# Kernel optimization log

Measured on AMD Instinct MI355X. Metric: run time of the kernel, lower is better.

The kernel has to match this reference:

```python
import jax, jax.numpy as jnp
import numpy as np

B, T, M, D, H, DFF = 8, 512, 64, 1024, 16, 4096
DH = D // H          # 64 head dim
ROT = DH // 2        # 32 rotary dims (int(head_dim*0.5))
ROPE_BASE = 10000.0
LN_EPS = 1e-5


def layernorm(x, g, b):
    mu = jnp.mean(x, -1, keepdims=True)
    var = jnp.mean(jnp.square(x - mu), -1, keepdims=True)
    return (x - mu) * jax.lax.rsqrt(var + LN_EPS) * g + b


def rotate_half(x):
    x1, x2 = x[..., : x.shape[-1] // 2], x[..., x.shape[-1] // 2:]
    return jnp.concatenate((-x2, x1), -1)


def setup_inputs() -> dict:
    key = jax.random.key(0)
    ks = jax.random.split(key, 8)
    s = 0.02
    return {
        "x": jax.random.normal(ks[0], (B, T, D), jnp.float32),
        "memory": jax.random.normal(ks[1], (B, M, D), jnp.float32),
        "Wq": jax.random.normal(ks[2], (D, D), jnp.float32) * s,
        "bq": jnp.zeros((D,), jnp.float32),
        "Wk": jax.random.normal(ks[3], (D, D), jnp.float32) * s,
        "bk": jnp.zeros((D,), jnp.float32),
        "Wv": jax.random.normal(ks[4], (D, D), jnp.float32) * s,
        "bv": jnp.zeros((D,), jnp.float32),
        "Wo": jax.random.normal(ks[5], (D, D), jnp.float32) * s,
        "bo": jnp.zeros((D,), jnp.float32),
        "W1": jax.random.normal(ks[6], (DFF, D), jnp.float32) * s,
        "b1": jnp.zeros((DFF,), jnp.float32),
        "W2": jax.random.normal(ks[7], (D, DFF), jnp.float32) * s,
        "b2": jnp.zeros((D,), jnp.float32),
        "g_attn": jnp.ones((D,), jnp.float32),
        "beta_attn": jnp.zeros((D,), jnp.float32),
        "g_mlp": jnp.ones((D,), jnp.float32),
        "beta_mlp": jnp.zeros((D,), jnp.float32),
    }


def reference(x, memory, Wq, bq, Wk, bk, Wv, bv, Wo, bo, W1, b1, W2, b2,
              g_attn, beta_attn, g_mlp, beta_mlp):
    L = M + T
    x_full = jnp.concatenate([memory, x], axis=1)            # (B, L, D)
    xa = layernorm(x_full, g_attn, beta_attn)

    def heads(t):  # (B, L, D) -> (B, H, L, DH)
        return t.reshape(B, L, H, DH).transpose(0, 2, 1, 3)

    q = heads(xa @ Wq.T + bq)
    k = heads(xa @ Wk.T + bk)
    v = heads(xa @ Wv.T + bv)

    # partial rotary embedding on first ROT dims
    inv_freq = 1.0 / (ROPE_BASE ** (jnp.arange(0, ROT, 2, dtype=jnp.float32) / ROT))
    freqs = jnp.arange(L, dtype=jnp.float32)[:, None] * inv_freq[None, :]  # (L, ROT/2)
    emb = jnp.concatenate((freqs, freqs), -1)                # (L, ROT)
    cos = jnp.cos(emb)[None, None]                           # (1,1,L,ROT)
    sin = jnp.sin(emb)[None, None]
    q_rot, q_pass = q[..., :ROT], q[..., ROT:]
    k_rot, k_pass = k[..., :ROT], k[..., ROT:]
    q_rot = q_rot * cos + rotate_half(q_rot) * sin
    k_rot = k_rot * cos + rotate_half(k_rot) * sin
    q = jnp.concatenate((q_rot, q_pass), -1)
    k = jnp.concatenate((k_rot, k_pass), -1)

    # prompt mask: memory rows attend memory only; target rows attend memory + causal target
    idx = jnp.arange(L)
    row, col = idx[:, None], idx[None, :]
    allowed = (col < M) | ((row >= M) & (col <= row))        # (L, L) bool

    scores = jnp.einsum('bhqd,bhkd->bhqk', q, k) / jnp.sqrt(jnp.float32(DH))
    scores = jnp.where(allowed[None, None], scores, jnp.float32(-1e30))
    attn = jax.nn.softmax(scores, axis=-1)
    o = jnp.einsum('bhqk,bhkd->bhqd', attn, v)
    o = o.transpose(0, 2, 1, 3).reshape(B, L, D)
    x_full = x_full + (o @ Wo.T + bo)

    xn = layernorm(x_full, g_mlp, beta_mlp)
    h = jnp.square(jax.nn.relu(xn @ W1.T + b1))              # ReLU^2 FFN
    x_full = x_full + (h @ W2.T + b2)
    return x_full[:, M:]
```

## Files before the change

kernel.cpp:

```cpp
#include <hip/hip_runtime.h>
#include <hip/hip_bf16.h>
#include <cmath>

using bf16 = __hip_bfloat16;
typedef __attribute__((ext_vector_type(8))) __bf16 bf16x8;
typedef __attribute__((ext_vector_type(4))) float f32x4;

struct __align__(8) bf16x4s { bf16 a, b, c, d; };

__device__ inline void gload_lds16(const void* g, void* l) {
  __builtin_amdgcn_global_load_lds(
      (__attribute__((address_space(1))) void*)g,
      (__attribute__((address_space(3))) void*)l, 16, 0, 0);
}

__device__ inline f32x4 mfma16(bf16x8 a, bf16x8 b, f32x4 c) {
  return __builtin_amdgcn_mfma_f32_16x16x32_bf16(a, b, c, 0, 0, 0);
}

#define BAR() __builtin_amdgcn_s_barrier()
#define VMC(N) asm volatile("s_waitcnt vmcnt(" #N ")" ::: "memory")
#define LGKM0() asm volatile("s_waitcnt lgkmcnt(0)" ::: "memory")

template<int MODE, int CHUNK>
__device__ __forceinline__ void gemm_body(
    const bf16* __restrict__ A, int lda, long sA,
    const bf16* __restrict__ B, int ldb, long sB,
    const float* __restrict__ bias,
    void* __restrict__ Out,
    int K, int ldo, long zstride,
    const float* __restrict__ rtab,
    bf16* __restrict__ o1, bf16* __restrict__ o2, bf16* __restrict__ o3)
{
  __shared__ bf16 lds[65536];
  const int tid = threadIdx.x, lane = tid & 63, wid = tid >> 6;
  const int wr = wid >> 2, wc = wid & 3;
  const int gx = gridDim.x;
  const int bidl = blockIdx.x + gx * blockIdx.y;
  const int xcd = bidl & 7, slot_ = bidl >> 3;
  int bx, by;
  if constexpr (CHUNK == 0) {
    const int sx = gx >> 2, sy = gridDim.y >> 1;
    bx = (xcd & 3) * sx + slot_ % sx;
    by = (xcd >> 2) * sy + slot_ / sx;
  } else {
    bx = slot_ % gx;
    by = xcd * (gridDim.y >> 3) + slot_ / gx;
  }
  const int m0 = by * 256, n0 = bx * 256;
  const int z = blockIdx.z;
  const bf16* Ab = A + (long)z * sA;
  const bf16* Bb = B + (long)z * sB;
  const int nt = K >> 6;

  f32x4 acc[8][4] = {};

  auto STAGE = [&](int par, int t, int part) {
    const bf16* src = (part < 2) ? Ab : Bb;
    const int ld = (part < 2) ? lda : ldb;
    const int rb = ((part < 2) ? m0 : n0) + (part & 1) * 128;
    const int k0 = t << 6;
    bf16* dst = &lds[(par * 4 + part) * 8192];
#pragma unroll
    for (int j = 0; j < 2; ++j) {
      int idx = j * 512 + tid;
      int row = idx >> 3;
      int ce = ((idx & 7) ^ (row & 7)) << 3;
      gload_lds16(src + (long)(rb + row) * ld + k0 + ce, dst + idx * 8);
    }
  };
  auto load_a = [&](bf16x8 (&a_)[4][2], int par, int mh) {
#pragma unroll
    for (int mf = 0; mf < 4; ++mf)
#pragma unroll
      for (int kk = 0; kk < 2; ++kk) {
        int r = mh * 64 + mf * 16 + (lane & 15);
        int cb = (kk * 64 + ((lane >> 4) << 4)) ^ ((r & 7) << 4);
        a_[mf][kk] = *(const bf16x8*)&lds[(par * 4 + wr) * 8192 + r * 64 + (cb >> 1)];
      }
  };
  auto load_b = [&](bf16x8 (&b_)[2][2], int par, int nh) {
#pragma unroll
    for (int nf = 0; nf < 2; ++nf)
#pragma unroll
      for (int kk = 0; kk < 2; ++kk) {
        int r = (wc & 1) * 64 + (nh * 2 + nf) * 16 + (lane & 15);
        int cb = (kk * 64 + ((lane >> 4) << 4)) ^ ((r & 7) << 4);
        b_[nf][kk] = *(const bf16x8*)&lds[(par * 4 + 2 + (wc >> 1)) * 8192 + r * 64 + (cb >> 1)];
      }
  };
  auto qmfma = [&](bf16x8 (&a_)[4][2], bf16x8 (&b_)[2][2], int mh, int nh) {
    __builtin_amdgcn_s_setprio(1);
#pragma unroll
    for (int kk = 0; kk < 2; ++kk)
#pragma unroll
      for (int mf = 0; mf < 4; ++mf)
#pragma unroll
        for (int nf = 0; nf < 2; ++nf)
          acc[mh * 4 + mf][nh * 2 + nf] =
              mfma16(a_[mf][kk], b_[nf][kk], acc[mh * 4 + mf][nh * 2 + nf]);
    __builtin_amdgcn_s_setprio(0);
  };

  STAGE(0, 0, 0); STAGE(0, 0, 1); STAGE(0, 0, 2); STAGE(0, 0, 3);
  STAGE(1, 1, 2); STAGE(1, 1, 0);
  VMC(4);
  BAR();

  const int half = nt >> 1;
  for (int i = 0; i < half; ++i) {
    const int u = 2 * i;
    const bool full = (i < half - 1);
    bf16x8 a[4][2], b0[2][2], b1[2][2];
    load_a(a, 0, 0); load_b(b0, 0, 0);
    STAGE(1, u + 1, 3);
    BAR();
    qmfma(a, b0, 0, 0);
    BAR();
    load_b(b1, 0, 1);
    STAGE(1, u + 1, 1);
    BAR();
    qmfma(a, b1, 0, 1);
    BAR();
    load_a(a, 0, 1);
    if (full) STAGE(0, u + 2, 2);
    BAR();
    qmfma(a, b1, 1, 1);
    BAR();
    if (full) STAGE(0, u + 2, 0);
    BAR();
    qmfma(a, b0, 1, 0);
    if (full) { VMC(4); } else { VMC(0); }
    BAR();
    load_a(a, 1, 0); load_b(b0, 1, 0);
    if (full) STAGE(0, u + 2, 3);
    BAR();
    qmfma(a, b0, 0, 0);
    BAR();
    load_b(b1, 1, 1);
    if (full) STAGE(0, u + 2, 1);
    BAR();
    qmfma(a, b1, 0, 1);
    BAR();
    load_a(a, 1, 1);
    if (full) STAGE(1, u + 3, 2);
    BAR();
    qmfma(a, b1, 1, 1);
    BAR();
    if (full) STAGE(1, u + 3, 0);
    BAR();
    qmfma(a, b0, 1, 0);
    if (full) VMC(4);
    BAR();
  }

  const int cb0 = n0 + wc * 64 + (lane & 15);
  const int rb0 = m0 + wr * 128 + ((lane >> 4) << 2);

  if constexpr (MODE == 9) {
    bf16* slot = &lds[wid * 8192];
    const int l15 = lane & 15;
    const int matq = n0 >> 10;
    const int hh = ((n0 & 1023) >> 6) + wc;
    const float b0v = bias[n0 + wc * 64 + l15];
    const float b1v = bias[n0 + wc * 64 + l15 + 16];
    const float b2v = bias[n0 + wc * 64 + l15 + 32];
    const float b3v = bias[n0 + wc * 64 + l15 + 48];
#pragma unroll
    for (int mf = 0; mf < 8; ++mf) {
#pragma unroll
      for (int j = 0; j < 4; ++j) {
        int lr = mf * 16 + ((lane >> 4) << 2) + j;
        float a0 = acc[mf][0][j] + b0v;
        float a1 = acc[mf][1][j] + b1v;
        float a2 = acc[mf][2][j] + b2v;
        float a3 = acc[mf][3][j] + b3v;
        if (matq < 2) {
          int rr = m0 + wr * 128 + lr;
          int p = rr % 576;
          float cs = rtab[p * 16 + l15];
          float sn = rtab[9216 + p * 16 + l15];
          float r0 = a0 * cs - a1 * sn;
          float r1 = a1 * cs + a0 * sn;
          a0 = r0; a1 = r1;
          if (matq == 0) {
            const float QS = 0.18033688011112043f;
            a0 *= QS; a1 *= QS; a2 *= QS; a3 *= QS;
          }
        }
        int sw = (lr & 7) << 3;
        slot[lr * 64 + ((l15) ^ sw)]      = __float2bfloat16(a0);
        slot[lr * 64 + ((l15 + 16) ^ sw)] = __float2bfloat16(a1);
        slot[lr * 64 + ((l15 + 32) ^ sw)] = __float2bfloat16(a2);
        slot[lr * 64 + ((l15 + 48) ^ sw)] = __float2bfloat16(a3);
      }
    }
    __syncthreads();
    if (matq == 2) {
#pragma unroll
      for (int it = 0; it < 16; ++it) {
        int pr0 = it * 8;
        bf16 tmp[8] __attribute__((aligned(16)));
#pragma unroll
        for (int j = 0; j < 8; ++j)
          tmp[j] = slot[(pr0 + j) * 64 + (lane ^ ((j & 7) << 3))];
        int rr = m0 + wr * 128 + pr0;
        int b_ = rr / 576, p = rr - b_ * 576;
        int zh = b_ * 16 + hh;
        *(bf16x8*)(o3 + (long)zh * 36864 + (long)lane * 576 + p) =
            *(const bf16x8*)tmp;
      }
    } else {
#pragma unroll
      for (int it = 0; it < 16; ++it) {
        int u = it * 64 + lane;
        int r_s = u >> 3, c_s = u & 7;
        int rr = m0 + wr * 128 + r_s;
        bf16x8 val = *(const bf16x8*)&slot[r_s * 64 + ((c_s ^ (r_s & 7)) << 3)];
        int b_ = rr / 576, p = rr - b_ * 576;
        int zh = b_ * 16 + hh;
        if (matq == 0) {
          if (p >= 64)
            *(bf16x8*)(o1 + ((long)zh * 512 + (p - 64)) * 64 + c_s * 8) = val;
        } else {
          *(bf16x8*)(o2 + ((long)zh * 576 + p) * 64 + c_s * 8) = val;
        }
      }
    }
  } else {
#pragma unroll
    for (int mf = 0; mf < 8; ++mf) {
#pragma unroll
      for (int nf = 0; nf < 4; ++nf) {
        int c = cb0 + nf * 16;
#pragma unroll
        for (int j = 0; j < 4; ++j) {
          int rr = rb0 + mf * 16 + j;
          float v = acc[mf][nf][j];
          if constexpr (MODE == 2) {
            float t2 = fmaxf(v + bias[c], 0.0f);
            ((bf16*)Out)[(long)rr * ldo + c] = __float2bfloat16(t2 * t2);
          } else {
            ((bf16*)Out)[(long)z * zstride + (long)rr * ldo + c] = __float2bfloat16(v);
          }
        }
      }
    }
  }
}

__global__ __launch_bounds__(512) void gemm_qkv(
    const bf16* A, const bf16* B, const float* bias, const float* rtab,
    bf16* o1, bf16* o2, bf16* o3)
{
  gemm_body<9, 0>(A, 1024, 0, B, 1024, 0, bias, nullptr, 1024, 0, 0,
                  rtab, o1, o2, o3);
}
__global__ __launch_bounds__(512) void gemm_wo(
    const bf16* A, const bf16* B, bf16* Out)
{
  gemm_body<8, 1>(A, 1024, 256, B, 1024, 256, nullptr, Out, 256, 1024,
                  4194304L, nullptr, nullptr, nullptr, nullptr);
}
__global__ __launch_bounds__(512) void gemm_w1(
    const bf16* A, const bf16* B, const float* bias, bf16* Out)
{
  gemm_body<2, 0>(A, 1024, 0, B, 1024, 0, bias, Out, 1024, 4096, 0,
                  nullptr, nullptr, nullptr, nullptr);
}
__global__ __launch_bounds__(512) void gemm_w2(
    const bf16* A, const bf16* B, bf16* Out)
{
  gemm_body<8, 1>(A, 4096, 1024, B, 4096, 1024, nullptr, Out, 1024, 1024,
                  4194304L, nullptr, nullptr, nullptr, nullptr);
}

__global__ __launch_bounds__(256) void reduce_k(
    const bf16* __restrict__ part, const float* __restrict__ bias,
    const bf16* __restrict__ resid, float* __restrict__ out)
{
  const int row = blockIdx.x, tid = threadIdx.x;
  const long rb = (long)row * 1024 + tid * 4;
  float a0 = 0, a1 = 0, a2 = 0, a3 = 0;
#pragma unroll
  for (int z = 0; z < 4; ++z) {
    bf16x4s t = *(const bf16x4s*)(part + (long)z * 4194304 + rb);
    a0 += __bfloat162float(t.a); a1 += __bfloat162float(t.b);
    a2 += __bfloat162float(t.c); a3 += __bfloat162float(t.d);
  }
  float4 b = ((const float4*)bias)[tid];
  bf16x4s r = *(const bf16x4s*)(resid + rb);
  float4 o;
  o.x = a0 + b.x + __bfloat162float(r.a);
  o.y = a1 + b.y + __bfloat162float(r.b);
  o.z = a2 + b.z + __bfloat162float(r.c);
  o.w = a3 + b.w + __bfloat162float(r.d);
  *(float4*)(out + rb) = o;
}

__global__ __launch_bounds__(256) void reduce_ln(
    const bf16* __restrict__ part, const float* __restrict__ bias,
    const float* __restrict__ resid, const float* __restrict__ g,
    const float* __restrict__ beta, bf16* __restrict__ x2,
    bf16* __restrict__ xn)
{
  const int row = blockIdx.x, tid = threadIdx.x;
  const long rb = (long)row * 1024 + tid * 4;
  float a0 = 0, a1 = 0, a2 = 0, a3 = 0;
#pragma unroll
  for (int z = 0; z < 4; ++z) {
    bf16x4s t = *(const bf16x4s*)(part + (long)z * 4194304 + rb);
    a0 += __bfloat162float(t.a); a1 += __bfloat162float(t.b);
    a2 += __bfloat162float(t.c); a3 += __bfloat162float(t.d);
  }
  float4 bb4 = ((const float4*)bias)[tid];
  float4 rr4 = *(const float4*)(resid + rb);
  float4 v;
  v.x = a0 + bb4.x + rr4.x; v.y = a1 + bb4.y + rr4.y;
  v.z = a2 + bb4.z + rr4.z; v.w = a3 + bb4.w + rr4.w;
  bf16x4s xo;
  xo.a = __float2bfloat16(v.x); xo.b = __float2bfloat16(v.y);
  xo.c = __float2bfloat16(v.z); xo.d = __float2bfloat16(v.w);
  *(bf16x4s*)(x2 + rb) = xo;

  float s = v.x + v.y + v.z + v.w;
  float s2 = v.x * v.x + v.y * v.y + v.z * v.z + v.w * v.w;
#pragma unroll
  for (int o = 32; o; o >>= 1) {
    s += __shfl_down(s, o);
    s2 += __shfl_down(s2, o);
  }
  __shared__ float red[8];
  const int w = tid >> 6, lane = tid & 63;
  if (lane == 0) { red[w] = s; red[4 + w] = s2; }
  __syncthreads();
  float S = red[0] + red[1] + red[2] + red[3];
  float S2 = red[4] + red[5] + red[6] + red[7];
  float mu = S * (1.0f / 1024.0f);
  float rs = rsqrtf(S2 * (1.0f / 1024.0f) - mu * mu + 1e-5f);
  float4 gg = ((const float4*)g)[tid];
  float4 be = ((const float4*)beta)[tid];
  bf16x4s o4;
  o4.a = __float2bfloat16((v.x - mu) * rs * gg.x + be.x);
  o4.b = __float2bfloat16((v.y - mu) * rs * gg.y + be.y);
  o4.c = __float2bfloat16((v.z - mu) * rs * gg.z + be.z);
  o4.d = __float2bfloat16((v.w - mu) * rs * gg.w + be.w);
  *(bf16x4s*)(xn + rb) = o4;
}

__global__ __launch_bounds__(256) void flash_attn(
    const bf16* __restrict__ qh, const bf16* __restrict__ kh,
    const bf16* __restrict__ vt, bf16* __restrict__ attn,
    const float* __restrict__ cWo, const float* __restrict__ cW1,
    const float* __restrict__ cW2, bf16* __restrict__ wrest)
{
  __shared__ bf16 ks[2][64 * 64];
  __shared__ bf16 vs[2][64 * 64];
  __shared__ bf16 pq[64 * 64];
  const int tid = threadIdx.x, lane = tid & 63, wv = tid >> 6;
  const int bid = blockIdx.x;

  if (bid >= 1024) {
    long e = (long)(bid - 1024) * 1024 + tid * 4;
    const long DD = 1048576, DF = 4194304;
    const float* src; long base;
    if (e < DD)           { src = cWo; base = 0; }
    else if (e < DD + DF) { src = cW1; base = DD; }
    else                  { src = cW2; base = DD + DF; }
    float4 v = *(const float4*)(src + (e - base));
    bf16x4s o4;
    o4.a = __float2bfloat16(v.x);
    o4.b = __float2bfloat16(v.y);
    o4.c = __float2bfloat16(v.z);
    o4.d = __float2bfloat16(v.w);
    *(bf16x4s*)(wrest + e) = o4;
    return;
  }

  const int xcd = bid & 7, sl = bid >> 3;
  const int zh = xcd * 16 + (sl >> 3);
  const int qt = sl & 7;
  const int b = zh >> 4, h = zh & 15;
  const int q0 = qt * 64;
  const bf16* qb = qh + (long)zh * 32768 + (long)q0 * 64;
  const bf16* kb = kh + (long)zh * 36864;
  const bf16* vb = vt + (long)zh * 36864;

#pragma unroll
  for (int i = 0; i < 2; ++i) {
    int idx = i * 256 + tid;
    int row = idx >> 3;
    int ce = ((idx & 7) ^ (row & 7)) << 3;
    gload_lds16(qb + (long)row * 64 + ce, pq + idx * 8);
  }
  auto stage_kv = [&](int bb, int j) {
#pragma unroll
    for (int it = 0; it < 2; ++it) {
      int idx = it * 256 + tid;
      int row = idx >> 3;
      int ce = ((idx & 7) ^ (row & 7)) << 3;
      gload_lds16(kb + (long)(j * 64 + row) * 64 + ce, &ks[bb][idx * 8]);
    }
#pragma unroll
    for (int it = 0; it < 2; ++it) {
      int idx = it * 256 + tid;
      int row = idx >> 3;
      int ce = ((idx & 7) ^ (row & 7)) << 3;
      gload_lds16(vb + (long)row * 576 + j * 64 + ce, &vs[bb][idx * 8]);
    }
  };
  stage_kv(0, 0);
  VMC(0);
  BAR();

  bf16x8 qf[2];
  {
    int r = wv * 16 + (lane & 15);
#pragma unroll
    for (int kk = 0; kk < 2; ++kk) {
      int c0 = kk * 32 + ((lane >> 4) << 3);
      qf[kk] = *(const bf16x8*)&pq[r * 64 + (c0 ^ ((r & 7) << 3))];
    }
  }

  f32x4 acc_o[4] = {};
  float mrun[4], lrun[4];
#pragma unroll
  for (int jj = 0; jj < 4; ++jj) { mrun[jj] = -1e30f; lrun[jj] = 0.0f; }

  const int nkv = qt + 2;
  int cur = 0;
  for (int j = 0; j < nkv; ++j) {
    if (j + 1 < nkv) stage_kv(cur ^ 1, j + 1);

    f32x4 sv[4] = {};
    __builtin_amdgcn_s_setprio(1);
#pragma unroll
    for (int kk = 0; kk < 2; ++kk) {
      bf16x8 kf[4];
      int c0 = kk * 32 + ((lane >> 4) << 3);
#pragma unroll
      for (int n = 0; n < 4; ++n) {
        int r = n * 16 + (lane & 15);
        kf[n] = *(const bf16x8*)&ks[cur][r * 64 + (c0 ^ ((r & 7) << 3))];
      }
#pragma unroll
      for (int n = 0; n < 4; ++n) sv[n] = mfma16(qf[kk], kf[n], sv[n]);
    }
    __builtin_amdgcn_s_setprio(0);

    if (j == nkv - 1) {
#pragma unroll
      for (int n = 0; n < 4; ++n) {
        int c = n * 16 + (lane & 15);
#pragma unroll
        for (int jj = 0; jj < 4; ++jj) {
          int r = wv * 16 + ((lane >> 4) << 2) + jj;
          if (c > r) sv[n][jj] = -1e30f;
        }
      }
    }
#pragma unroll
    for (int jj = 0; jj < 4; ++jj) {
      float pm = fmaxf(fmaxf(sv[0][jj], sv[1][jj]), fmaxf(sv[2][jj], sv[3][jj]));
#pragma unroll
      for (int off = 1; off < 16; off <<= 1) pm = fmaxf(pm, __shfl_xor(pm, off));
      float mnew = fmaxf(mrun[jj], pm);
      float sc = exp2f(mrun[jj] - mnew);
      mrun[jj] = mnew;
      float rs = 0.0f;
#pragma unroll
      for (int n = 0; n < 4; ++n) {
        float p = exp2f(sv[n][jj] - mnew);
        sv[n][jj] = p;
        rs += p;
      }
#pragma unroll
      for (int off = 1; off < 16; off <<= 1) rs += __shfl_xor(rs, off);
      lrun[jj] = lrun[jj] * sc + rs;
#pragma unroll
      for (int nd = 0; nd < 4; ++nd) acc_o[nd][jj] *= sc;
    }
#pragma unroll
    for (int n = 0; n < 4; ++n)
#pragma unroll
      for (int jj = 0; jj < 4; ++jj) {
        int pr = wv * 16 + ((lane >> 4) << 2) + jj;
        int pc = n * 16 + (lane & 15);
        pq[pr * 64 + (pc ^ ((pr & 7) << 3))] = __float2bfloat16(sv[n][jj]);
      }
    __builtin_amdgcn_s_setprio(1);
#pragma unroll
    for (int kk = 0; kk < 2; ++kk) {
      int c0 = kk * 32 + ((lane >> 4) << 3);
      bf16x8 pa, vf[4];
      {
        int r = wv * 16 + (lane & 15);
        pa = *(const bf16x8*)&pq[r * 64 + (c0 ^ ((r & 7) << 3))];
      }
#pragma unroll
      for (int nd = 0; nd < 4; ++nd) {
        int r = nd * 16 + (lane & 15);
        vf[nd] = *(const bf16x8*)&vs[cur][r * 64 + (c0 ^ ((r & 7) << 3))];
      }
#pragma unroll
      for (int nd = 0; nd < 4; ++nd) acc_o[nd] = mfma16(pa, vf[nd], acc_o[nd]);
    }
    __builtin_amdgcn_s_setprio(0);

    if (j + 1 < nkv) {
      LGKM0();
      VMC(0);
      BAR();
      cur ^= 1;
    }
  }
  bf16* ob = attn + ((long)b * 512 + q0) * 1024 + h * 64;
#pragma unroll
  for (int jj = 0; jj < 4; ++jj) {
    float inv = 1.0f / lrun[jj];
    int r = wv * 16 + ((lane >> 4) << 2) + jj;
#pragma unroll
    for (int nd = 0; nd < 4; ++nd)
      ob[(long)r * 1024 + nd * 16 + (lane & 15)] = __float2bfloat16(acc_o[nd][jj] * inv);
  }
}

__global__ __launch_bounds__(256) void ln_setup(
    const float* __restrict__ xin, const float* __restrict__ mem,
    const float* __restrict__ g, const float* __restrict__ beta,
    bf16* __restrict__ xa,
    const float* __restrict__ wq, const float* __restrict__ wk,
    const float* __restrict__ wv,
    const float* __restrict__ bq, const float* __restrict__ bk,
    const float* __restrict__ bv,
    bf16* __restrict__ wout, float* __restrict__ bout,
    float* __restrict__ tab)
{
  const int blk = blockIdx.x, tid = threadIdx.x;
  if (blk >= 4608) {
    if (blk < 7680) {
      long e = (long)(blk - 4608) * 1024 + tid * 4;
      const long DD = 1048576;
      const float* src; long base;
      if (e < DD)          { src = wq; base = 0; }
      else if (e < 2 * DD) { src = wk; base = DD; }
      else                 { src = wv; base = 2 * DD; }
      float4 v = *(const float4*)(src + (e - base));
      bf16x4s o4;
      o4.a = __float2bfloat16(v.x);
      o4.b = __float2bfloat16(v.y);
      o4.c = __float2bfloat16(v.z);
      o4.d = __float2bfloat16(v.w);
      *(bf16x4s*)(wout + e) = o4;
    } else if (blk < 7692) {
      int i = (blk - 7680) * 256 + tid;
      if (i < 1024)      bout[i] = bq[i];
      else if (i < 2048) bout[i] = bk[i - 1024];
      else if (i < 3072) bout[i] = bv[i - 2048];
    } else {
      int i = (blk - 7692) * 256 + tid;
      if (i < 9216) {
        int p = i >> 4, f = i & 15;
        float invf = expf(-(float)f * 0.5756462732485114f);
        float ang = (float)p * invf;
        tab[i] = cosf(ang);
        tab[9216 + i] = sinf(ang);
      }
    }
    return;
  }
  const int row = blk;
  int b = row / 576, p = row % 576;
  const float* src = (p < 64) ? (mem + ((long)b * 64 + p) * 1024)
                              : (xin + ((long)b * 512 + (p - 64)) * 1024);
  float4 v = ((const float4*)src)[tid];
  float s = v.x + v.y + v.z + v.w;
  float s2 = v.x * v.x + v.y * v.y + v.z * v.z + v.w * v.w;
#pragma unroll
  for (int o = 32; o; o >>= 1) {
    s += __shfl_down(s, o);
    s2 += __shfl_down(s2, o);
  }
  __shared__ float red[8];
  const int w = tid >> 6, lane = tid & 63;
  if (lane == 0) { red[w] = s; red[4 + w] = s2; }
  __syncthreads();
  float S = red[0] + red[1] + red[2] + red[3];
  float S2 = red[4] + red[5] + red[6] + red[7];
  float mu = S * (1.0f / 1024.0f);
  float rs = rsqrtf(S2 * (1.0f / 1024.0f) - mu * mu + 1e-5f);
  float4 gg = ((const float4*)g)[tid];
  float4 bb = ((const float4*)beta)[tid];
  bf16x4s o4;
  o4.a = __float2bfloat16((v.x - mu) * rs * gg.x + bb.x);
  o4.b = __float2bfloat16((v.y - mu) * rs * gg.y + bb.y);
  o4.c = __float2bfloat16((v.z - mu) * rs * gg.z + bb.z);
  o4.d = __float2bfloat16((v.w - mu) * rs * gg.w + bb.w);
  *(bf16x4s*)(xa + (long)row * 1024 + tid * 4) = o4;
}

extern "C" void kernel_launch(void* const* d_in, const int* in_sizes, int n_in,
                              void* d_out, int out_size, void* d_ws, size_t ws_size,
                              hipStream_t stream)
{
  (void)in_sizes; (void)n_in; (void)out_size; (void)ws_size;
  const float* x    = (const float*)d_in[0];
  const float* mem  = (const float*)d_in[1];
  const float* Wq   = (const float*)d_in[2];
  const float* bq   = (const float*)d_in[3];
  const float* Wk   = (const float*)d_in[4];
  const float* bk   = (const float*)d_in[5];
  const float* Wv   = (const float*)d_in[6];
  const float* bv   = (const float*)d_in[7];
  const float* Wo   = (const float*)d_in[8];
  const float* bo   = (const float*)d_in[9];
  const float* W1   = (const float*)d_in[10];
  const float* b1   = (const float*)d_in[11];
  const float* W2   = (const float*)d_in[12];
  const float* b2   = (const float*)d_in[13];
  const float* g_a  = (const float*)d_in[14];
  const float* bt_a = (const float*)d_in[15];
  const float* g_m  = (const float*)d_in[16];
  const float* bt_m = (const float*)d_in[17];
  float* out = (float*)d_out;

  char* ws = (char*)d_ws;
  size_t off = 0;
  auto carve = [&](size_t bytes) -> void* {
    void* p = ws + off;
    off = (off + bytes + 255) & ~(size_t)255;
    return p;
  };
  bf16*  wB    = (bf16*)carve(12582912L * 2);
  float* bqkv  = (float*)carve(3072 * 4);
  float* rtab  = (float*)carve(9216 * 2 * 4);
  bf16*  xa    = (bf16*)carve(4608L * 1024 * 2);
  bf16*  qh    = (bf16*)carve(8L * 16 * 512 * 64 * 2);
  bf16*  kh    = (bf16*)carve(8L * 16 * 576 * 64 * 2);
  bf16*  vt    = (bf16*)carve(8L * 16 * 576 * 64 * 2);
  bf16*  attn  = (bf16*)carve(4096L * 1024 * 2);
  bf16*  x2    = (bf16*)carve(4096L * 1024 * 2);
  bf16*  xn    = (bf16*)carve(4096L * 1024 * 2);
  bf16*  hbuf  = (bf16*)carve(4096L * 4096 * 2);
  bf16*  partsb= (bf16*)carve(4L * 4096 * 1024 * 2);

  ln_setup<<<7728, 256, 0, stream>>>(x, mem, g_a, bt_a, xa,
                                     Wq, Wk, Wv, bq, bk, bv, wB, bqkv, rtab);

  gemm_qkv<<<dim3(12, 18, 1), 512, 0, stream>>>(xa, wB, bqkv, rtab, qh, kh, vt);

  flash_attn<<<10240, 256, 0, stream>>>(qh, kh, vt, attn,
                                        Wo, W1, W2, wB + 3145728L);

  gemm_wo<<<dim3(4, 16, 4), 512, 0, stream>>>(attn, wB + 3145728L, partsb);
  reduce_ln<<<4096, 256, 0, stream>>>(partsb, bo, x, g_m, bt_m, x2, xn);

  gemm_w1<<<dim3(16, 16, 1), 512, 0, stream>>>(xn, wB + 4194304L, b1, hbuf);

  gemm_w2<<<dim3(4, 16, 4), 512, 0, stream>>>(hbuf, wB + 8388608L, partsb);
  reduce_k<<<4096, 256, 0, stream>>>(partsb, b2, x2, out);
}
```

Measured before the change: 196.2 us.

## Double flash-attention query tile to 128 rows with 512-thread blocks

The flash attention kernel now processes 128 query rows per block using 8 waves instead of 64 rows with 4 waves, so each staged K/V tile is reused by twice as many waves. This halves the number of attention blocks and the total K/V traffic from global memory. The causal mask now covers the last two KV tiles with absolute indices, and the weight-conversion tail blocks are resized to match. The cost is coarser work granularity and more uneven per-block work, since the number of KV iterations now grows as 2*qt+3.

```diff
diff --git a/kernel.cpp b/kernel.cpp
--- a/kernel.cpp
+++ b/kernel.cpp
@@ -348,7 +348,7 @@
   *(bf16x4s*)(xn + rb) = o4;
 }
 
-__global__ __launch_bounds__(256) void flash_attn(
+__global__ __launch_bounds__(512) void flash_attn(
     const bf16* __restrict__ qh, const bf16* __restrict__ kh,
     const bf16* __restrict__ vt, bf16* __restrict__ attn,
     const float* __restrict__ cWo, const float* __restrict__ cW1,
@@ -356,12 +356,12 @@
 {
   __shared__ bf16 ks[2][64 * 64];
   __shared__ bf16 vs[2][64 * 64];
-  __shared__ bf16 pq[64 * 64];
+  __shared__ bf16 pq[128 * 64];
   const int tid = threadIdx.x, lane = tid & 63, wv = tid >> 6;
   const int bid = blockIdx.x;
 
-  if (bid >= 1024) {
-    long e = (long)(bid - 1024) * 1024 + tid * 4;
+  if (bid >= 512) {
+    long e = (long)(bid - 512) * 2048 + tid * 4;
     const long DD = 1048576, DF = 4194304;
     const float* src; long base;
     if (e < DD)           { src = cWo; base = 0; }
@@ -378,35 +378,31 @@
   }
 
   const int xcd = bid & 7, sl = bid >> 3;
-  const int zh = xcd * 16 + (sl >> 3);
-  const int qt = sl & 7;
+  const int zh = xcd * 16 + (sl >> 2);
+  const int qt = sl & 3;
   const int b = zh >> 4, h = zh & 15;
-  const int q0 = qt * 64;
+  const int q0 = qt * 128;
   const bf16* qb = qh + (long)zh * 32768 + (long)q0 * 64;
   const bf16* kb = kh + (long)zh * 36864;
   const bf16* vb = vt + (long)zh * 36864;
 
 #pragma unroll
   for (int i = 0; i < 2; ++i) {
-    int idx = i * 256 + tid;
+    int idx = i * 512 + tid;
     int row = idx >> 3;
     int ce = ((idx & 7) ^ (row & 7)) << 3;
     gload_lds16(qb + (long)row * 64 + ce, pq + idx * 8);
   }
   auto stage_kv = [&](int bb, int j) {
-#pragma unroll
-    for (int it = 0; it < 2; ++it) {
-      int idx = it * 256 + tid;
-      int row = idx >> 3;
-      int ce = ((idx & 7) ^ (row & 7)) << 3;
-      gload_lds16(kb + (long)(j * 64 + row) * 64 + ce, &ks[bb][idx * 8]);
-    }
-#pragma unroll
-    for (int it = 0; it < 2; ++it) {
-      int idx = it * 256 + tid;
-      int row = idx >> 3;
-      int ce = ((idx & 7) ^ (row & 7)) << 3;
-      gload_lds16(vb + (long)row * 576 + j * 64 + ce, &vs[bb][idx * 8]);
+    {
+      int row = tid >> 3;
+      int ce = ((tid & 7) ^ (row & 7)) << 3;
+      gload_lds16(kb + (long)(j * 64 + row) * 64 + ce, &ks[bb][tid * 8]);
+    }
+    {
+      int row = tid >> 3;
+      int ce = ((tid & 7) ^ (row & 7)) << 3;
+      gload_lds16(vb + (long)row * 576 + j * 64 + ce, &vs[bb][tid * 8]);
     }
   };
   stage_kv(0, 0);
@@ -428,7 +424,7 @@
 #pragma unroll
   for (int jj = 0; jj < 4; ++jj) { mrun[jj] = -1e30f; lrun[jj] = 0.0f; }
 
-  const int nkv = qt + 2;
+  const int nkv = 2 * qt + 3;
   int cur = 0;
   for (int j = 0; j < nkv; ++j) {
     if (j + 1 < nkv) stage_kv(cur ^ 1, j + 1);
@@ -449,14 +445,14 @@
     }
     __builtin_amdgcn_s_setprio(0);
 
-    if (j == nkv - 1) {
+    if (j >= nkv - 2) {
 #pragma unroll
       for (int n = 0; n < 4; ++n) {
-        int c = n * 16 + (lane & 15);
+        int c = j * 64 + n * 16 + (lane & 15);
 #pragma unroll
         for (int jj = 0; jj < 4; ++jj) {
-          int r = wv * 16 + ((lane >> 4) << 2) + jj;
-          if (c > r) sv[n][jj] = -1e30f;
+          int r = q0 + wv * 16 + ((lane >> 4) << 2) + jj;
+          if (c > r + 64) sv[n][jj] = -1e30f;
         }
       }
     }
@@ -650,8 +646,8 @@
 
   gemm_qkv<<<dim3(12, 18, 1), 512, 0, stream>>>(xa, wB, bqkv, rtab, qh, kh, vt);
 
-  flash_attn<<<10240, 256, 0, stream>>>(qh, kh, vt, attn,
-                                        Wo, W1, W2, wB + 3145728L);
+  flash_attn<<<5120, 512, 0, stream>>>(qh, kh, vt, attn,
+                                       Wo, W1, W2, wB + 3145728L);
 
   gemm_wo<<<dim3(4, 16, 4), 512, 0, stream>>>(attn, wB + 3145728L, partsb);
   reduce_ln<<<4096, 256, 0, stream>>>(partsb, bo, x, g_m, bt_m, x2, xn);
```

Result: no change. 198.2 us (+1.0%).
